# Optimization experiments

Hardware: AMD Instinct MI355X
Metric: run time of the kernel (lower is better)

The kernel has to match this reference:

```python
import jax, jax.numpy as jnp
import numpy as np
from jax import lax

B0, C0, H0, W0 = 4, 128, 48, 48
GR = 32  # growth rate
NL = 4   # dense layers


def conv1x1(x, w, b):
    # w: [O, Cin], x: [B, Cin, H, W]
    return jnp.einsum('oc,bchw->bohw', w, x) + b[None, :, None, None]


def conv3x3(x, w, b):
    y = lax.conv_general_dilated(x, w, (1, 1), [(1, 1), (1, 1)],
                                 dimension_numbers=('NCHW', 'OIHW', 'NCHW'))
    return y + b[None, :, None, None]


def batchnorm(x, g, b, eps=1e-5):
    # training-mode BatchNorm2d: batch statistics over (B, H, W)
    mu = jnp.mean(x, axis=(0, 2, 3), keepdims=True)
    var = jnp.var(x, axis=(0, 2, 3), keepdims=True)
    return (x - mu) * lax.rsqrt(var + eps) * g[None, :, None, None] + b[None, :, None, None]


def apply_rope(x):
    B, C, H, W = x.shape
    half = C // 2
    theta = 1.0 / (10000.0 ** (jnp.arange(half, dtype=x.dtype) / half))
    # pos_emb[h, w, j] = (h + w) * theta[j]
    pos = (jnp.arange(H, dtype=x.dtype)[:, None, None]
           + jnp.arange(W, dtype=x.dtype)[None, :, None]) * theta
    cos = jnp.cos(pos).transpose(2, 0, 1)  # [half, H, W]
    sin = jnp.sin(pos).transpose(2, 0, 1)
    xr = x.reshape(B, half, 2, H, W)
    x_re, x_im = xr[:, :, 0], xr[:, :, 1]
    rr = x_re * cos - x_im * sin
    ri = x_re * sin + x_im * cos
    return jnp.stack([rr, ri], axis=2).reshape(B, C, H, W)


def setup_inputs() -> dict:
    key = jax.random.key(0)
    ks = iter(jax.random.split(key, 64))
    def nrm(shape, s=0.05):
        return jax.random.normal(next(ks), shape, jnp.float32) * s
    C = C0
    dc = C + NL * GR  # 256 dense-block output channels
    hid = 4 * C
    d = {
        'x': jax.random.normal(next(ks), (B0, C0, H0, W0), jnp.float32),
        'r_w': nrm((C, C)), 'r_b': jnp.zeros((C,), jnp.float32),
        'k_w': nrm((C, C)), 'k_b': jnp.zeros((C,), jnp.float32),
        'v_w': nrm((C, C)), 'v_b': jnp.zeros((C,), jnp.float32),
        'wc1_w': nrm((C // 4, C, 3, 3)), 'wc1_b': jnp.zeros((C // 4,), jnp.float32),
        'wc2_w': nrm((C, C // 4)), 'wc2_b': jnp.zeros((C,), jnp.float32),
        'u': nrm((C,), 0.1),
        'sn1_w': nrm((dc // 4, dc)), 'sn1_b': jnp.zeros((dc // 4,), jnp.float32),
        'sn2_w': nrm((dc, dc // 4)), 'sn2_b': jnp.zeros((dc,), jnp.float32),
        'lb_w': nrm((C // 4, dc)), 'lb_b': jnp.zeros((C // 4,), jnp.float32),
        'ld_w': nrm((C // 4, dc)), 'ld_b': jnp.zeros((C // 4,), jnp.float32),
        'ps_w': nrm((C, C // 4)), 'ps_b': jnp.zeros((C,), jnp.float32),
        'pq_w': nrm((C, C)), 'pq_b': jnp.zeros((C,), jnp.float32),
        'fc1_w': nrm((hid, C)), 'fc1_b': jnp.zeros((hid,), jnp.float32),
        'fc2_w': nrm((C, hid)), 'fc2_b': jnp.zeros((C,), jnp.float32),
    }
    for i in range(NL):
        cin = C + i * GR
        d[f'db_g{i}'] = jnp.ones((cin,), jnp.float32)
        d[f'db_b{i}'] = jnp.zeros((cin,), jnp.float32)
        d[f'db_w{i}'] = nrm((GR, cin, 3, 3))
        d[f'db_cb{i}'] = jnp.zeros((GR,), jnp.float32)
    return d


def _forward(x, r_w, r_b, k_w, k_b, v_w, v_b, wc1_w, wc1_b, wc2_w, wc2_b, u,
             db_g0, db_b0, db_w0, db_cb0, db_g1, db_b1, db_w1, db_cb1,
             db_g2, db_b2, db_w2, db_cb2, db_g3, db_b3, db_w3, db_cb3,
             sn1_w, sn1_b, sn2_w, sn2_b, lb_w, lb_b, ld_w, ld_b,
             ps_w, ps_b, pq_w, pq_b, fc1_w, fc1_b, fc2_w, fc2_b):
    B, C, H, W = x.shape
    N = H * W
    # decay gate w (hidden is None so it multiplies zeros, kept for fidelity)
    w_gate = jax.nn.sigmoid(conv1x1(jax.nn.relu(conv3x3(x, wc1_w, wc1_b)), wc2_w, wc2_b)).reshape(B, C, N)
    x_rope = apply_rope(x)
    r = jax.nn.sigmoid(conv1x1(x, r_w, r_b))
    k = conv1x1(x_rope, k_w, k_b).reshape(B, C, N)
    v = conv1x1(x_rope, v_w, v_b).reshape(B, C, N)
    zeros = jnp.zeros_like(k)
    new_num = zeros * jnp.exp(-w_gate) + k * v
    new_den = zeros * jnp.exp(-w_gate) + k
    eu = jnp.exp(u)[None, :, None]
    wkv = ((new_num + eu * k * v) / (new_den + eu * k)).reshape(B, C, H, W)
    recursive_output = r * wkv
    # dense block (concat-growth)
    feats = x
    for g, bb, wt, cb in ((db_g0, db_b0, db_w0, db_cb0), (db_g1, db_b1, db_w1, db_cb1),
                          (db_g2, db_b2, db_w2, db_cb2), (db_g3, db_b3, db_w3, db_cb3)):
        h = jax.nn.relu(batchnorm(feats, g, bb))
        feats = jnp.concatenate([feats, conv3x3(h, wt, cb)], axis=1)
    df = feats  # [B, C+4*GR, H, W]
    # adaptive spiking neuron
    tau = jnp.mean(jax.nn.sigmoid(conv1x1(jax.nn.relu(conv1x1(df, sn1_w, sn1_b)), sn2_w, sn2_b)),
                   axis=(2, 3), keepdims=True)
    spike_prob = jax.nn.sigmoid((df - 1.0) * 5.0)
    sf = spike_prob * (df * jnp.exp(-1.0 / (tau + 1e-6))) + (1.0 - spike_prob) * df
    # first attention over N tokens, channels = C//4
    Bf = conv1x1(sf, lb_w, lb_b).reshape(B, -1, N)
    Df = conv1x1(sf, ld_w, ld_b).reshape(B, -1, N)
    attn = jax.nn.softmax(jnp.einsum('bcn,bcm->bnm', Bf, Bf), axis=-1)
    att1 = jnp.einsum('bnm,bcm->bcn', attn, Df).reshape(B, -1, H, W)
    spike_output = conv1x1(att1, ps_w, ps_b)
    combined = recursive_output + spike_output
    # second attention (k/v convs are shared with WKV path)
    Q = conv1x1(combined, pq_w, pq_b).reshape(B, C, N)
    K = conv1x1(combined, k_w, k_b).reshape(B, C, N)
    V = conv1x1(combined, v_w, v_b).reshape(B, C, N)
    scores = jnp.einsum('bcn,bcm->bnm', Q, K) / jnp.sqrt(jnp.asarray(C, x.dtype))
    aw = jax.nn.softmax(scores, axis=-1)
    att2 = jnp.einsum('bnm,bcm->bcn', aw, V).reshape(B, C, H, W)
    x1 = x + att2
    out = x1 + conv1x1(jax.nn.relu(conv1x1(x1, fc1_w, fc1_b)) ** 2, fc2_w, fc2_b)
    return out, new_num, new_den


def reference(x, r_w, r_b, k_w, k_b, v_w, v_b, wc1_w, wc1_b, wc2_w, wc2_b, u,
              db_g0, db_b0, db_w0, db_cb0, db_g1, db_b1, db_w1, db_cb1,
              db_g2, db_b2, db_w2, db_cb2, db_g3, db_b3, db_w3, db_cb3,
              sn1_w, sn1_b, sn2_w, sn2_b, lb_w, lb_b, ld_w, ld_b,
              ps_w, ps_b, pq_w, pq_b, fc1_w, fc1_b, fc2_w, fc2_b):
    return _forward(x, r_w, r_b, k_w, k_b, v_w, v_b, wc1_w, wc1_b, wc2_w, wc2_b, u,
                    db_g0, db_b0, db_w0, db_cb0, db_g1, db_b1, db_w1, db_cb1,
                    db_g2, db_b2, db_w2, db_cb2, db_g3, db_b3, db_w3, db_cb3,
                    sn1_w, sn1_b, sn2_w, sn2_b, lb_w, lb_b, ld_w, ld_b,
                    ps_w, ps_b, pq_w, pq_b, fc1_w, fc1_b, fc2_w, fc2_b)
```

## Files before the change

kernel.cpp:

```cpp
#include <hip/hip_runtime.h>
#include <math.h>

#define BB 4
#define CC 128
#define HH 48
#define WW 48
#define NSP (HH*WW)
#define DCC 256
#define BCN (BB*CC*NSP)
#define KS 4

typedef float f32x4 __attribute__((ext_vector_type(4)));
typedef __bf16 bf16x8 __attribute__((ext_vector_type(8)));
typedef __bf16 bf16x4 __attribute__((ext_vector_type(4)));

__device__ __forceinline__ float sigmf(float v) { return 1.0f / (1.0f + __expf(-v)); }

struct Prep {
  const float* wsrc[13];
  int wlen[13];
  int woff[13];
  const float* psrc[4];
  int pcin[4];
  int poff[4];
  const float* x;
  float* sums;
  float* sums2;
  __bf16* x_t;
  __bf16* xrope_t;
};
__global__ __launch_bounds__(256) void prep_kernel(Prep a, __bf16* __restrict__ wdst,
                                                   __bf16* __restrict__ pdst) {
  __shared__ float lds[32][33];
  __shared__ float rs[4], rs2[4];
  int g = blockIdx.y;
  int idx = blockIdx.x * 256 + threadIdx.x;
  if (g < 13) {
    if (idx < a.wlen[g]) wdst[a.woff[g] + idx] = (__bf16)a.wsrc[g][idx];
  } else if (g < 17) {
    int L = g - 13;
    int cin = a.pcin[L];
    if (idx < 9 * 32 * cin) {
      int c = idx % cin;
      int o = (idx / cin) % 32;
      int tap = idx / (cin * 32);
      pdst[a.poff[L] + idx] = (__bf16)a.psrc[L][((size_t)o * cin + c) * 9 + tap];
    }
  } else if (g == 17) {
    int c = blockIdx.x;
    if (c >= 128) return;
    float s = 0.f, s2 = 0.f;
    for (int i = threadIdx.x; i < BB * NSP; i += 256) {
      int b = i / NSP, n = i % NSP;
      float v = a.x[((size_t)b * 128 + c) * NSP + n];
      s += v;
      s2 += v * v;
    }
#pragma unroll
    for (int off = 32; off > 0; off >>= 1) {
      s += __shfl_down(s, off);
      s2 += __shfl_down(s2, off);
    }
    int wid = threadIdx.x >> 6;
    if ((threadIdx.x & 63) == 0) { rs[wid] = s; rs2[wid] = s2; }
    __syncthreads();
    if (threadIdx.x == 0) {
      a.sums[c] = rs[0] + rs[1] + rs[2] + rs[3];
      a.sums2[c] = rs2[0] + rs2[1] + rs2[2] + rs2[3];
    }
  } else {
    int T = (g - 18) * 256 + blockIdx.x;
    if (T >= 1152) return;
    int b = T / 288;
    int r = T % 288;
    int c0 = (r / 72) * 32;
    int n0 = (r % 72) * 32;
    int tid = threadIdx.x;
    int nn = tid & 31, cs = tid >> 5;
#pragma unroll
    for (int j = 0; j < 4; ++j) {
      int cc = c0 + cs * 4 + j;
      lds[cs * 4 + j][nn] = a.x[((size_t)b * 128 + cc) * NSP + n0 + nn];
    }
    __syncthreads();
    int c = tid & 31, ns = tid >> 5;
#pragma unroll
    for (int j = 0; j < 4; ++j) {
      int n2 = ns * 4 + j;
      float pv = lds[c][n2];
      a.x_t[((size_t)b * NSP + n0 + n2) * 128 + c0 + c] = (__bf16)pv;
      int gc = c0 + c;
      int i = gc >> 1;
      float re = lds[c & ~1][n2];
      float im = lds[c | 1][n2];
      int n = n0 + n2;
      int h = n / WW, w = n % WW;
      float theta = __expf(-9.2103403719761836f * ((float)i) / 64.0f);
      float pos = (float)(h + w) * theta;
      float cs_ = cosf(pos), sn_ = sinf(pos);
      float vr_ = (gc & 1) ? (re * sn_ + im * cs_) : (re * cs_ - im * sn_);
      a.xrope_t[((size_t)b * NSP + n0 + n2) * 128 + c0 + c] = (__bf16)vr_;
    }
  }
}

__global__ __launch_bounds__(256) void kvr_kernel(
    const __bf16* __restrict__ xrope_t, const __bf16* __restrict__ x_t,
    const __bf16* __restrict__ wk, const __bf16* __restrict__ wvp,
    const __bf16* __restrict__ wr,
    const float* __restrict__ k_b, const float* __restrict__ v_b,
    const float* __restrict__ r_b, const float* __restrict__ u,
    float* __restrict__ kden, float* __restrict__ knum, float* __restrict__ rec) {
  int tid = threadIdx.x;
  int wv = tid >> 6, lane = tid & 63;
  int m15 = lane & 15, quad = lane >> 4;
  int b = blockIdx.y;
  int n0 = blockIdx.x * 16;
  int o0 = wv * 32;
  int n = n0 + m15;
  const __bf16* brr = xrope_t + ((size_t)b * NSP + n) * 128 + quad * 8;
  const __bf16* brx = x_t + ((size_t)b * NSP + n) * 128 + quad * 8;
  const __bf16* ak0 = wk + (size_t)(o0 + m15) * 128 + quad * 8;
  const __bf16* ak1 = wk + (size_t)(o0 + 16 + m15) * 128 + quad * 8;
  const __bf16* av0 = wvp + (size_t)(o0 + m15) * 128 + quad * 8;
  const __bf16* av1 = wvp + (size_t)(o0 + 16 + m15) * 128 + quad * 8;
  const __bf16* ar0 = wr + (size_t)(o0 + m15) * 128 + quad * 8;
  const __bf16* ar1 = wr + (size_t)(o0 + 16 + m15) * 128 + quad * 8;
  f32x4 fk[2], fv[2], fr[2];
#pragma unroll
  for (int t = 0; t < 2; ++t) {
    fk[t] = (f32x4){0.f, 0.f, 0.f, 0.f};
    fv[t] = (f32x4){0.f, 0.f, 0.f, 0.f};
    fr[t] = (f32x4){0.f, 0.f, 0.f, 0.f};
  }
#pragma unroll
  for (int kc = 0; kc < 128; kc += 32) {
    bf16x8 br_ = *(const bf16x8*)(brr + kc);
    bf16x8 bx_ = *(const bf16x8*)(brx + kc);
    fk[0] = __builtin_amdgcn_mfma_f32_16x16x32_bf16(*(const bf16x8*)(ak0 + kc), br_, fk[0], 0, 0, 0);
    fk[1] = __builtin_amdgcn_mfma_f32_16x16x32_bf16(*(const bf16x8*)(ak1 + kc), br_, fk[1], 0, 0, 0);
    fv[0] = __builtin_amdgcn_mfma_f32_16x16x32_bf16(*(const bf16x8*)(av0 + kc), br_, fv[0], 0, 0, 0);
    fv[1] = __builtin_amdgcn_mfma_f32_16x16x32_bf16(*(const bf16x8*)(av1 + kc), br_, fv[1], 0, 0, 0);
    fr[0] = __builtin_amdgcn_mfma_f32_16x16x32_bf16(*(const bf16x8*)(ar0 + kc), bx_, fr[0], 0, 0, 0);
    fr[1] = __builtin_amdgcn_mfma_f32_16x16x32_bf16(*(const bf16x8*)(ar1 + kc), bx_, fr[1], 0, 0, 0);
  }
#pragma unroll
  for (int t = 0; t < 2; ++t) {
#pragma unroll
    for (int reg = 0; reg < 4; ++reg) {
      int ol = o0 + t * 16 + quad * 4 + reg;
      float kk = fk[t][reg] + k_b[ol];
      float vv = fv[t][reg] + v_b[ol];
      float rr = sigmf(fr[t][reg] + r_b[ol]);
      float eu = __expf(u[ol]);
      size_t idx = ((size_t)b * 128 + ol) * NSP + n;
      float nv = kk * vv, tt = eu * kk;
      kden[idx] = kk;
      knum[idx] = nv;
      rec[idx] = rr * ((nv + tt * vv) / (kk + tt));
    }
  }
}

template <int OUT>
__device__ __forceinline__ void gemm_store(void* outp, int b, int n, int Oseg,
                                           int obase, int quad, const float* vr) {
  if (OUT == 0) {
    float* op = (float*)outp;
#pragma unroll
    for (int reg = 0; reg < 4; ++reg)
      op[((size_t)b * Oseg + obase + quad * 4 + reg) * NSP + n] = vr[reg];
  } else if (OUT == 1) {
    __bf16* op = (__bf16*)outp;
    bf16x4 pk;
#pragma unroll
    for (int reg = 0; reg < 4; ++reg) pk[reg] = (__bf16)vr[reg];
    *(bf16x4*)(op + ((size_t)b * NSP + n) * Oseg + obase + quad * 4) = pk;
  } else {
    __bf16* op = (__bf16*)outp;
#pragma unroll
    for (int reg = 0; reg < 4; ++reg)
      op[((size_t)b * Oseg + obase + quad * 4 + reg) * NSP + n] = (__bf16)vr[reg];
  }
}

template <int K, int ACT, int OUT0, int OUT1, int OUT2, int SPLITB>
__global__ __launch_bounds__(256) void gemm_mfma_kernel(
    const __bf16* __restrict__ in_t, const __bf16* __restrict__ in_t2,
    const __bf16* __restrict__ wb,
    const float* __restrict__ bias0, const float* __restrict__ bias1,
    const float* __restrict__ bias2,
    const float* __restrict__ add0, const float* __restrict__ add1,
    void* __restrict__ out0, void* __restrict__ out1, void* __restrict__ out2,
    int osplit, int osplit2, int Ototal, float sc0, float sc1, float sc2) {
  int tid = threadIdx.x;
  int wv = tid >> 6, lane = tid & 63;
  int m15 = lane & 15, quad = lane >> 4;
  int b = blockIdx.y;
  int n0 = blockIdx.x * 16;
  int wpb = blockDim.x >> 6;
  int o0 = (blockIdx.z * wpb + wv) * 32;
  if (o0 >= Ototal) return;
  int n = n0 + m15;
  const __bf16* brow = in_t + ((size_t)b * NSP + n) * (SPLITB ? 128 : K) + quad * 8;
  const __bf16* brow2 = SPLITB ? (in_t2 + ((size_t)b * NSP + n) * 128 + quad * 8) : nullptr;
  const __bf16* a0p = wb + (size_t)(o0 + m15) * K + quad * 8;
  const __bf16* a1p = wb + (size_t)(o0 + 16 + m15) * K + quad * 8;
  f32x4 of0 = (f32x4){0.f, 0.f, 0.f, 0.f};
  f32x4 of1 = (f32x4){0.f, 0.f, 0.f, 0.f};
#pragma unroll
  for (int kc = 0; kc < K; kc += 32) {
    bf16x8 bfr;
    if constexpr (SPLITB) {
      bfr = (kc < 128) ? *(const bf16x8*)(brow + kc) : *(const bf16x8*)(brow2 + (kc - 128));
    } else {
      bfr = *(const bf16x8*)(brow + kc);
    }
    bf16x8 a0 = *(const bf16x8*)(a0p + kc);
    bf16x8 a1 = *(const bf16x8*)(a1p + kc);
    of0 = __builtin_amdgcn_mfma_f32_16x16x32_bf16(a0, bfr, of0, 0, 0, 0);
    of1 = __builtin_amdgcn_mfma_f32_16x16x32_bf16(a1, bfr, of1, 0, 0, 0);
  }
  int seg = (o0 >= osplit2) ? 2 : (o0 >= osplit) ? 1 : 0;
  int segb = (seg == 2) ? osplit2 : (seg == 1) ? osplit : 0;
  int sege = (seg == 2) ? Ototal : (seg == 1) ? osplit2 : osplit;
  int Oseg = sege - segb;
  int ol0 = o0 - segb;
  const float* bias = (seg == 2) ? bias2 : (seg == 1) ? bias1 : bias0;
  const float* add = (seg == 2) ? nullptr : (seg == 1) ? add1 : add0;
  void* outp = (seg == 2) ? out2 : (seg == 1) ? out1 : out0;
  float sc = (seg == 2) ? sc2 : (seg == 1) ? sc1 : sc0;
#pragma unroll
  for (int t = 0; t < 2; ++t) {
    f32x4 acc = t ? of1 : of0;
    float vr[4];
#pragma unroll
    for (int reg = 0; reg < 4; ++reg) {
      int ol = ol0 + t * 16 + quad * 4 + reg;
      float v = acc[reg] + bias[ol];
      if (ACT == 1) v = fmaxf(v, 0.0f);
      else if (ACT == 2) v = sigmf(v);
      else if (ACT == 3) { v = fmaxf(v, 0.0f); v = v * v; }
      v *= sc;
      if (add) v += add[((size_t)b * Oseg + ol) * NSP + n];
      vr[reg] = v;
    }
    if constexpr (OUT0 == 3) {
#pragma unroll
      for (int reg = 0; reg < 4; ++reg) {
        float sv = vr[reg];
        sv += __shfl_xor(sv, 1);
        sv += __shfl_xor(sv, 2);
        sv += __shfl_xor(sv, 4);
        sv += __shfl_xor(sv, 8);
        if (m15 == 0)
          ((float*)out0)[((size_t)(b * DCC + ol0 + t * 16 + quad * 4 + reg)) * 144 +
                         blockIdx.x] = sv;
      }
    } else {
      if (seg == 0) gemm_store<OUT0>(outp, b, n, Oseg, ol0 + t * 16, quad, vr);
      else if (seg == 1) gemm_store<OUT1>(outp, b, n, Oseg, ol0 + t * 16, quad, vr);
      else gemm_store<OUT2>(outp, b, n, Oseg, ol0 + t * 16, quad, vr);
    }
  }
}

__global__ __launch_bounds__(128) void lbld_sf_kernel(
    const __bf16* __restrict__ x_t, const __bf16* __restrict__ dense_t,
    const float* __restrict__ taupart, const __bf16* __restrict__ wlb,
    const float* __restrict__ lb_b, const float* __restrict__ ld_b,
    __bf16* __restrict__ Bft, __bf16* __restrict__ Dfb) {
  __shared__ float ef[256];
  int tid = threadIdx.x;
  int b = blockIdx.y;
  for (int ch = tid; ch < 256; ch += 128) {
    const f32x4* tp = (const f32x4*)(taupart + ((size_t)(b * DCC + ch)) * 144);
    f32x4 s4 = (f32x4){0.f, 0.f, 0.f, 0.f};
#pragma unroll
    for (int j = 0; j < 36; ++j) s4 += tp[j];
    float tv = (s4.x + s4.y + s4.z + s4.w) * (1.0f / (float)NSP);
    ef[ch] = __expf(-1.0f / (tv + 1e-6f)) - 1.0f;
  }
  __syncthreads();
  int wv = tid >> 6, lane = tid & 63;
  int m15 = lane & 15, quad = lane >> 4;
  int n0 = blockIdx.x * 16;
  int o0 = wv * 32;
  int n = n0 + m15;
  const __bf16* bx = x_t + ((size_t)b * NSP + n) * 128 + quad * 8;
  const __bf16* bd = dense_t + ((size_t)b * NSP + n) * 128 + quad * 8;
  const __bf16* a0p = wlb + (size_t)(o0 + m15) * 256 + quad * 8;
  const __bf16* a1p = wlb + (size_t)(o0 + 16 + m15) * 256 + quad * 8;
  f32x4 of0 = (f32x4){0.f, 0.f, 0.f, 0.f};
  f32x4 of1 = (f32x4){0.f, 0.f, 0.f, 0.f};
#pragma unroll
  for (int kc = 0; kc < 256; kc += 32) {
    bf16x8 raw = (kc < 128) ? *(const bf16x8*)(bx + kc) : *(const bf16x8*)(bd + (kc - 128));
    bf16x8 sfv;
#pragma unroll
    for (int j = 0; j < 8; ++j) {
      float df = (float)raw[j];
      float sp = sigmf((df - 1.0f) * 5.0f);
      sfv[j] = (__bf16)(df * (1.0f + sp * ef[kc + quad * 8 + j]));
    }
    bf16x8 a0 = *(const bf16x8*)(a0p + kc);
    bf16x8 a1 = *(const bf16x8*)(a1p + kc);
    of0 = __builtin_amdgcn_mfma_f32_16x16x32_bf16(a0, sfv, of0, 0, 0, 0);
    of1 = __builtin_amdgcn_mfma_f32_16x16x32_bf16(a1, sfv, of1, 0, 0, 0);
  }
  if (o0 == 0) {
#pragma unroll
    for (int t = 0; t < 2; ++t) {
      f32x4 acc = t ? of1 : of0;
      bf16x4 pk;
#pragma unroll
      for (int reg = 0; reg < 4; ++reg) pk[reg] = (__bf16)(acc[reg] + lb_b[t * 16 + quad * 4 + reg]);
      *(bf16x4*)(Bft + ((size_t)b * NSP + n) * 32 + t * 16 + quad * 4) = pk;
    }
  } else {
#pragma unroll
    for (int t = 0; t < 2; ++t) {
      f32x4 acc = t ? of1 : of0;
#pragma unroll
      for (int reg = 0; reg < 4; ++reg) {
        int ol = t * 16 + quad * 4 + reg;
        Dfb[((size_t)b * 32 + ol) * NSP + n] = (__bf16)(acc[reg] + ld_b[ol]);
      }
    }
  }
}

template <int Cin>
__global__ __launch_bounds__(256) void convbn_kernel(
    const __bf16* __restrict__ x_t, const __bf16* __restrict__ dense_t,
    const __bf16* __restrict__ wb, const float* __restrict__ cb,
    float* __restrict__ sums, float* __restrict__ sums2,
    const float* __restrict__ cpart_in,
    const float* __restrict__ g, const float* __restrict__ bbp,
    __bf16* __restrict__ dense_out, float* __restrict__ cpart_out, int cout0) {
  constexpr int KCin = Cin / 32;
  constexpr int NIT = 9 * KCin;
  __shared__ float red[4][64][8];
  __shared__ float scsh[2][Cin];
  __shared__ float tred[64][4];
  __shared__ float fin[64];
  int tid = threadIdx.x;
  const float inv = 1.0f / (float)(BB * NSP);

  if (cpart_in) {
    int row = tid >> 2, sl = tid & 3;
    const f32x4* cp = (const f32x4*)(cpart_in + (size_t)row * 576 + sl * 144);
    f32x4 s4 = (f32x4){0.f, 0.f, 0.f, 0.f};
#pragma unroll
    for (int j = 0; j < 36; ++j) s4 += cp[j];
    tred[row][sl] = s4.x + s4.y + s4.z + s4.w;
    __syncthreads();
    if (tid < 64) fin[tid] = tred[tid][0] + tred[tid][1] + tred[tid][2] + tred[tid][3];
    __syncthreads();
    if (blockIdx.x == 0 && blockIdx.y == 0 && tid < 32) {
      sums[Cin - 32 + tid] = fin[tid];
      sums2[Cin - 32 + tid] = fin[32 + tid];
    }
  }
  for (int ch = tid; ch < Cin; ch += 256) {
    float S, S2;
    if (cpart_in && ch >= Cin - 32) {
      S = fin[ch - (Cin - 32)];
      S2 = fin[ch - (Cin - 32) + 32];
    } else {
      S = sums[ch];
      S2 = sums2[ch];
    }
    float m = S * inv;
    float var = S2 * inv - m * m;
    float sc_ = rsqrtf(var + 1e-5f) * g[ch];
    scsh[0][ch] = sc_;
    scsh[1][ch] = bbp[ch] - m * sc_;
  }
  __syncthreads();

  int wv = tid >> 6, lane = tid & 63;
  int m15 = lane & 15, quad = lane >> 4;
  int b = blockIdx.y;
  int n0 = blockIdx.x * 16;
  int n = n0 + m15;
  int h = n / WW, w = n % WW;
  f32x4 of0 = (f32x4){0.f, 0.f, 0.f, 0.f};
  f32x4 of1 = (f32x4){0.f, 0.f, 0.f, 0.f};
  const __bf16* bx_ = x_t + (size_t)b * NSP * 128;
  const __bf16* bd_ = dense_t + (size_t)b * NSP * 128;
  const bf16x8 zf = {};
  int begin = (wv * NIT) / 4, end = ((wv + 1) * NIT) / 4;
  int cur = -1;
  float bsc[8], bsh[8];
  const __bf16* base = nullptr;
  for (int ci = begin; ci < end; ++ci) {
    int chunk = ci / 9;
    int tap = ci - chunk * 9;
    int kc = chunk * 32;
    if (chunk != cur) {
      cur = chunk;
      int cc = kc + quad * 8;
#pragma unroll
      for (int j = 0; j < 8; ++j) {
        bsc[j] = scsh[0][cc + j];
        bsh[j] = scsh[1][cc + j];
      }
      base = (cc < 128) ? (bx_ + cc) : (bd_ + cc - 128);
    }
    int dh = tap / 3 - 1, dw = tap % 3 - 1;
    bool valid = ((unsigned)(h + dh) < HH) && ((unsigned)(w + dw) < WW);
    int pa = valid ? (n + dh * WW + dw) : 0;
    bf16x8 raw = *(const bf16x8*)(base + (size_t)pa * 128);
    bf16x8 bfr;
#pragma unroll
    for (int j = 0; j < 8; ++j) {
      float v = fmaxf((float)raw[j] * bsc[j] + bsh[j], 0.0f);
      bfr[j] = (__bf16)v;
    }
    if (!valid) bfr = zf;
    const __bf16* wt = wb + (size_t)tap * 32 * Cin + kc + quad * 8;
    bf16x8 a0 = *(const bf16x8*)(wt + (size_t)m15 * Cin);
    bf16x8 a1 = *(const bf16x8*)(wt + (size_t)(16 + m15) * Cin);
    of0 = __builtin_amdgcn_mfma_f32_16x16x32_bf16(a0, bfr, of0, 0, 0, 0);
    of1 = __builtin_amdgcn_mfma_f32_16x16x32_bf16(a1, bfr, of1, 0, 0, 0);
  }
  float* myred = red[wv][lane];
#pragma unroll
  for (int reg = 0; reg < 4; ++reg) {
    myred[reg] = of0[reg];
    myred[4 + reg] = of1[reg];
  }
  __syncthreads();
  if (wv == 0) {
    int dloc = cout0 - 128;
    __bf16* dt = dense_out + ((size_t)b * NSP + n) * 128 + dloc;
    bf16x4 pk0, pk1;
    float sv[4][4];
#pragma unroll
    for (int reg = 0; reg < 4; ++reg) {
      int o = quad * 4 + reg;
      float v0 = red[0][lane][reg] + red[1][lane][reg] + red[2][lane][reg] +
                 red[3][lane][reg] + cb[o];
      float v1 = red[0][lane][4 + reg] + red[1][lane][4 + reg] + red[2][lane][4 + reg] +
                 red[3][lane][4 + reg] + cb[16 + o];
      pk0[reg] = (__bf16)v0;
      pk1[reg] = (__bf16)v1;
      sv[reg][0] = v0;
      sv[reg][1] = v0 * v0;
      sv[reg][2] = v1;
      sv[reg][3] = v1 * v1;
    }
    *(bf16x4*)(dt + quad * 4) = pk0;
    *(bf16x4*)(dt + 16 + quad * 4) = pk1;
    if (cpart_out) {
#pragma unroll
      for (int reg = 0; reg < 4; ++reg) {
        float a0 = sv[reg][0], q0 = sv[reg][1], a1 = sv[reg][2], q1 = sv[reg][3];
#pragma unroll
        for (int mk = 1; mk < 16; mk <<= 1) {
          a0 += __shfl_xor(a0, mk);
          q0 += __shfl_xor(q0, mk);
          a1 += __shfl_xor(a1, mk);
          q1 += __shfl_xor(q1, mk);
        }
        if (m15 == 0) {
          int o = quad * 4 + reg;
          int pidx = blockIdx.y * 144 + blockIdx.x;
          cpart_out[(size_t)o * 576 + pidx] = a0;
          cpart_out[(size_t)(32 + o) * 576 + pidx] = q0;
          cpart_out[(size_t)(16 + o) * 576 + pidx] = a1;
          cpart_out[(size_t)(48 + o) * 576 + pidx] = q1;
        }
      }
    }
  }
}

template <int CD>
__global__ __launch_bounds__(256) void attn_part_kernel(
    const __bf16* __restrict__ Qt, const __bf16* __restrict__ Kt,
    const __bf16* __restrict__ Vb, __bf16* __restrict__ Op,
    float* __restrict__ lp) {
  constexpr int NC = CD / 16;
  constexpr int KC = CD / 32;
  constexpr int KEYS = NSP / KS;
  constexpr int KP = CD + 4;
  constexpr int VP = 36;
  __shared__ __bf16 kl[32][KP];
  __shared__ __bf16 vl[CD][VP];
  __shared__ float pt[4][16][36];
  int tid = threadIdx.x;
  int wv = tid >> 6, lane = tid & 63;
  int m15 = lane & 15, quad = lane >> 4;
  int b = blockIdx.y, ks = blockIdx.z;
  int n0 = blockIdx.x * 64 + wv * 16;

  bf16x8 qf[KC];
  const __bf16* qrow = Qt + ((size_t)b * NSP + n0 + m15) * CD + quad * 8;
#pragma unroll
  for (int kc = 0; kc < KC; ++kc) qf[kc] = *(const bf16x8*)(qrow + kc * 32);

  f32x4 of[NC];
#pragma unroll
  for (int i = 0; i < NC; ++i) of[i] = (f32x4){0.f, 0.f, 0.f, 0.f};
  float l0 = 0.f, l1 = 0.f, l2 = 0.f, l3 = 0.f;

  const __bf16* Kb = Kt + (size_t)b * NSP * CD;
  const __bf16* Vbb = Vb + (size_t)b * CD * NSP;
  float(*ptw)[36] = pt[wv];

  for (int m0 = ks * KEYS; m0 < (ks + 1) * KEYS; m0 += 32) {
    __syncthreads();
    for (int i = tid; i < 32 * CD / 8; i += 256) {
      int row = i / (CD / 8);
      int cc8 = (i % (CD / 8)) * 8;
      *(bf16x8*)&kl[row][cc8] = *(const bf16x8*)(Kb + (size_t)(m0 + row) * CD + cc8);
    }
    for (int i = tid; i < CD * 4; i += 256) {
      int ch = i / 4;
      int k8 = (i % 4) * 8;
      *(bf16x8*)&vl[ch][k8] = *(const bf16x8*)(Vbb + (size_t)ch * NSP + m0 + k8);
    }
    __syncthreads();
    f32x4 s[2];
#pragma unroll
    for (int t = 0; t < 2; ++t) {
      f32x4 acc = (f32x4){0.f, 0.f, 0.f, 0.f};
#pragma unroll
      for (int kc = 0; kc < KC; ++kc) {
        bf16x8 kf = *(const bf16x8*)&kl[t * 16 + m15][kc * 32 + quad * 8];
        acc = __builtin_amdgcn_mfma_f32_16x16x32_bf16(qf[kc], kf, acc, 0, 0, 0);
      }
      s[t] = acc;
    }
#pragma unroll
    for (int t = 0; t < 2; ++t) {
      float e0 = __expf(s[t].x), e1 = __expf(s[t].y), e2 = __expf(s[t].z), e3 = __expf(s[t].w);
      l0 += e0; l1 += e1; l2 += e2; l3 += e3;
      ptw[quad * 4 + 0][t * 16 + m15] = e0;
      ptw[quad * 4 + 1][t * 16 + m15] = e1;
      ptw[quad * 4 + 2][t * 16 + m15] = e2;
      ptw[quad * 4 + 3][t * 16 + m15] = e3;
    }
    const float* prow = &ptw[m15][quad * 8];
    f32x4 pa = *(const f32x4*)(prow);
    f32x4 pb = *(const f32x4*)(prow + 4);
    bf16x8 pf;
    pf[0] = (__bf16)pa.x; pf[1] = (__bf16)pa.y; pf[2] = (__bf16)pa.z; pf[3] = (__bf16)pa.w;
    pf[4] = (__bf16)pb.x; pf[5] = (__bf16)pb.y; pf[6] = (__bf16)pb.z; pf[7] = (__bf16)pb.w;
#pragma unroll
    for (int ct = 0; ct < NC; ++ct) {
      bf16x8 vf = *(const bf16x8*)&vl[ct * 16 + m15][quad * 8];
      of[ct] = __builtin_amdgcn_mfma_f32_16x16x32_bf16(pf, vf, of[ct], 0, 0, 0);
    }
  }

#pragma unroll
  for (int off = 1; off < 16; off <<= 1) {
    l0 += __shfl_xor(l0, off);
    l1 += __shfl_xor(l1, off);
    l2 += __shfl_xor(l2, off);
    l3 += __shfl_xor(l3, off);
  }
  float* lpb = lp + (size_t)(ks * BB + b) * NSP + n0;
  if (m15 == 0) {
    lpb[quad * 4 + 0] = l0;
    lpb[quad * 4 + 1] = l1;
    lpb[quad * 4 + 2] = l2;
    lpb[quad * 4 + 3] = l3;
  }
  __bf16* Ob = Op + (size_t)(ks * BB + b) * CD * NSP;
#pragma unroll
  for (int ct = 0; ct < NC; ++ct) {
    bf16x4 pk;
#pragma unroll
    for (int reg = 0; reg < 4; ++reg) pk[reg] = (__bf16)of[ct][reg];
    *(bf16x4*)(Ob + (size_t)(ct * 16 + m15) * NSP + n0 + quad * 4) = pk;
  }
}

__global__ __launch_bounds__(256) void combine32_kernel(const __bf16* __restrict__ Op,
                                                        const float* __restrict__ lp,
                                                        __bf16* __restrict__ att1_t) {
  __shared__ float lds[32][33];
  int b = blockIdx.z;
  int n0 = blockIdx.x * 32;
  int tid = threadIdx.x;
  int nn = tid & 31, cs = tid >> 5;
  float ltot = 0.f;
#pragma unroll
  for (int ks = 0; ks < KS; ++ks) ltot += lp[(size_t)(ks * BB + b) * NSP + n0 + nn];
  float linv = 1.0f / ltot;
#pragma unroll
  for (int j = 0; j < 4; ++j) {
    int cc = cs * 4 + j;
    float s = 0.f;
#pragma unroll
    for (int ks = 0; ks < KS; ++ks)
      s += (float)Op[((size_t)(ks * BB + b) * 32 + cc) * NSP + n0 + nn];
    lds[cc][nn] = s * linv;
  }
  __syncthreads();
  int c = tid & 31, ns = tid >> 5;
#pragma unroll
  for (int j = 0; j < 4; ++j) {
    int n2 = ns * 4 + j;
    att1_t[((size_t)b * NSP + n0 + n2) * 32 + c] = (__bf16)lds[c][n2];
  }
}

__global__ __launch_bounds__(256) void combine128_kernel(
    const __bf16* __restrict__ Op, const float* __restrict__ lp,
    const float* __restrict__ x, float* __restrict__ x1, __bf16* __restrict__ x1_t) {
  __shared__ float lds[32][33];
  int b = blockIdx.z;
  int n0 = blockIdx.x * 32;
  int c0 = blockIdx.y * 32;
  int tid = threadIdx.x;
  int nn = tid & 31, cs = tid >> 5;
  float ltot = 0.f;
#pragma unroll
  for (int ks = 0; ks < KS; ++ks) ltot += lp[(size_t)(ks * BB + b) * NSP + n0 + nn];
  float linv = 1.0f / ltot;
#pragma unroll
  for (int j = 0; j < 4; ++j) {
    int gc = c0 + cs * 4 + j;
    float s = 0.f;
#pragma unroll
    for (int ks = 0; ks < KS; ++ks)
      s += (float)Op[((size_t)(ks * BB + b) * CC + gc) * NSP + n0 + nn];
    float v = s * linv + x[((size_t)b * CC + gc) * NSP + n0 + nn];
    lds[cs * 4 + j][nn] = v;
    x1[((size_t)b * CC + gc) * NSP + n0 + nn] = v;
  }
  __syncthreads();
  int c = tid & 31, ns = tid >> 5;
#pragma unroll
  for (int j = 0; j < 4; ++j) {
    int n2 = ns * 4 + j;
    x1_t[((size_t)b * NSP + n0 + n2) * CC + c0 + c] = (__bf16)lds[c][n2];
  }
}

extern "C" void kernel_launch(void* const* d_in, const int* in_sizes, int n_in,
                              void* d_out, int out_size, void* d_ws, size_t ws_size,
                              hipStream_t stream) {
  const float* x = (const float*)d_in[0];
  const float* r_w = (const float*)d_in[1];
  const float* r_b = (const float*)d_in[2];
  const float* k_w = (const float*)d_in[3];
  const float* k_b = (const float*)d_in[4];
  const float* v_w = (const float*)d_in[5];
  const float* v_b = (const float*)d_in[6];
  const float* u = (const float*)d_in[11];
  const float* sn1_w = (const float*)d_in[12];
  const float* sn1_b = (const float*)d_in[13];
  const float* sn2_w = (const float*)d_in[14];
  const float* sn2_b = (const float*)d_in[15];
  const float* lb_w = (const float*)d_in[16];
  const float* lb_b = (const float*)d_in[17];
  const float* ld_w = (const float*)d_in[18];
  const float* ld_b = (const float*)d_in[19];
  const float* ps_w = (const float*)d_in[20];
  const float* ps_b = (const float*)d_in[21];
  const float* pq_w = (const float*)d_in[22];
  const float* pq_b = (const float*)d_in[23];
  const float* fc1_w = (const float*)d_in[24];
  const float* fc1_b = (const float*)d_in[25];
  const float* fc2_w = (const float*)d_in[26];
  const float* fc2_b = (const float*)d_in[27];
  const float* db_g[4] = {(const float*)d_in[28], (const float*)d_in[32],
                          (const float*)d_in[36], (const float*)d_in[40]};
  const float* db_b[4] = {(const float*)d_in[29], (const float*)d_in[33],
                          (const float*)d_in[37], (const float*)d_in[41]};
  const float* db_w[4] = {(const float*)d_in[30], (const float*)d_in[34],
                          (const float*)d_in[38], (const float*)d_in[42]};
  const float* db_cb[4] = {(const float*)d_in[31], (const float*)d_in[35],
                           (const float*)d_in[39], (const float*)d_in[43]};

  float* outp = (float*)d_out;
  float* knum = outp + BCN;
  float* kden = outp + 2 * (size_t)BCN;

  float* ws = (float*)d_ws;
  const size_t F_FEATS = 0;
  const size_t F_REC = 4718592;
  const size_t F_V = 5898240;
  const size_t F_R = 7077888;
  const size_t F_XR = 8257536;
  const size_t F_XT = 8847360;
  const size_t F_DFB = 9437184;
  const size_t F_AT1T = 9584640;
  const size_t F_CT = 9732096;
  const size_t F_LP = 10321920;
  const size_t F_WB = 10434048;
  const size_t F_WB3 = 10575360;
  const size_t F_STATS = 10676736;
  const size_t F_TAUP = 10714112;
  float* sums = ws + F_STATS;
  float* sums2 = ws + F_STATS + 256;
  float* cpart0 = ws + F_FEATS;
  float* cpart1 = cpart0 + 36864;
  float* cpart2 = cpart1 + 36864;
  float* taupart = ws + F_TAUP;
  float* lp = ws + F_LP;
  __bf16* wbase = (__bf16*)(ws + F_WB);
  __bf16* wb3 = (__bf16*)(ws + F_WB3);
  const int W_KV = 0;
  const int W_R = 32768;
  const int W_SN1 = 49152;
  const int W_SN2 = 65536;
  const int W_LBLD = 81920;
  const int W_PS = 98304;
  const int W_PQK = 102400;
  const int W_FC1 = 151552;
  const int W_FC2 = 217088;
  const int W3_OFF[4] = {0, 36864, 82944, 138240};

  dim3 blk(256);
  __bf16* xrope_t = (__bf16*)(ws + F_XR);
  __bf16* x_t = (__bf16*)(ws + F_XT);

  Prep pp;
  pp.wsrc[0] = k_w;    pp.wlen[0] = 16384; pp.woff[0] = W_KV;
  pp.wsrc[1] = v_w;    pp.wlen[1] = 16384; pp.woff[1] = W_KV + 16384;
  pp.wsrc[2] = r_w;    pp.wlen[2] = 16384; pp.woff[2] = W_R;
  pp.wsrc[3] = sn1_w;  pp.wlen[3] = 16384; pp.woff[3] = W_SN1;
  pp.wsrc[4] = sn2_w;  pp.wlen[4] = 16384; pp.woff[4] = W_SN2;
  pp.wsrc[5] = lb_w;   pp.wlen[5] = 8192;  pp.woff[5] = W_LBLD;
  pp.wsrc[6] = ld_w;   pp.wlen[6] = 8192;  pp.woff[6] = W_LBLD + 8192;
  pp.wsrc[7] = ps_w;   pp.wlen[7] = 4096;  pp.woff[7] = W_PS;
  pp.wsrc[8] = pq_w;   pp.wlen[8] = 16384; pp.woff[8] = W_PQK;
  pp.wsrc[9] = k_w;    pp.wlen[9] = 16384; pp.woff[9] = W_PQK + 16384;
  pp.wsrc[10] = v_w;   pp.wlen[10] = 16384; pp.woff[10] = W_PQK + 32768;
  pp.wsrc[11] = fc1_w; pp.wlen[11] = 65536; pp.woff[11] = W_FC1;
  pp.wsrc[12] = fc2_w; pp.wlen[12] = 65536; pp.woff[12] = W_FC2;
  for (int i = 0; i < 4; ++i) {
    pp.psrc[i] = db_w[i];
    pp.pcin[i] = 128 + 32 * i;
    pp.poff[i] = W3_OFF[i];
  }
  pp.x = x;
  pp.sums = sums;
  pp.sums2 = sums2;
  pp.x_t = x_t;
  pp.xrope_t = xrope_t;
  prep_kernel<<<dim3(256, 23), blk, 0, stream>>>(pp, wbase, wb3);

  kvr_kernel<<<dim3(144, 4), blk, 0, stream>>>(
      xrope_t, x_t, wbase + W_KV, wbase + W_KV + 16384, wbase + W_R,
      k_b, v_b, r_b, u, kden, knum, ws + F_REC);

  __bf16* dense_t = (__bf16*)(ws + F_R);
  convbn_kernel<128><<<dim3(144, 4), blk, 0, stream>>>(
      x_t, dense_t, wb3 + W3_OFF[0], db_cb[0], sums, sums2, nullptr,
      db_g[0], db_b[0], dense_t, cpart0, 128);
  convbn_kernel<160><<<dim3(144, 4), blk, 0, stream>>>(
      x_t, dense_t, wb3 + W3_OFF[1], db_cb[1], sums, sums2, cpart0,
      db_g[1], db_b[1], dense_t, cpart1, 160);
  convbn_kernel<192><<<dim3(144, 4), blk, 0, stream>>>(
      x_t, dense_t, wb3 + W3_OFF[2], db_cb[2], sums, sums2, cpart1,
      db_g[2], db_b[2], dense_t, cpart2, 192);
  convbn_kernel<224><<<dim3(144, 4), blk, 0, stream>>>(
      x_t, dense_t, wb3 + W3_OFF[3], db_cb[3], sums, sums2, cpart2,
      db_g[3], db_b[3], dense_t, nullptr, 224);

  __bf16* z1_t = (__bf16*)(ws + F_XR);
  gemm_mfma_kernel<256, 1, 1, 1, 0, 1><<<dim3(144, 4, 1), dim3(128), 0, stream>>>(
      x_t, dense_t, wbase + W_SN1, sn1_b, sn1_b, nullptr, nullptr, nullptr,
      z1_t, z1_t, nullptr, 64, 64, 64, 1.f, 1.f, 1.f);
  gemm_mfma_kernel<64, 2, 3, 3, 0, 0><<<dim3(144, 4, 2), blk, 0, stream>>>(
      z1_t, nullptr, wbase + W_SN2, sn2_b, sn2_b, nullptr, nullptr, nullptr,
      taupart, taupart, nullptr, 256, 256, 256, 1.f, 1.f, 1.f);
  __bf16* Bft = (__bf16*)(ws + F_CT + 294912);
  __bf16* Dfb = (__bf16*)(ws + F_DFB);
  lbld_sf_kernel<<<dim3(144, 4), dim3(128), 0, stream>>>(
      x_t, dense_t, taupart, wbase + W_LBLD, lb_b, ld_b, Bft, Dfb);
  __bf16* Opart = (__bf16*)(ws + F_FEATS);
  attn_part_kernel<32><<<dim3(36, 4, KS), blk, 0, stream>>>(Bft, Bft, Dfb, Opart, lp);
  __bf16* att1_t = (__bf16*)(ws + F_AT1T);
  combine32_kernel<<<dim3(72, 1, 4), blk, 0, stream>>>(Opart, lp, att1_t);
  __bf16* comb_t = (__bf16*)(ws + F_CT);
  gemm_mfma_kernel<32, 0, 1, 1, 0, 0><<<dim3(144, 4, 1), blk, 0, stream>>>(
      att1_t, nullptr, wbase + W_PS, ps_b, ps_b, nullptr, ws + F_REC, ws + F_REC,
      comb_t, comb_t, nullptr, 128, 128, 128, 1.f, 1.f, 1.f);

  __bf16* Qt = (__bf16*)(ws + F_XR);
  __bf16* K2t = (__bf16*)(ws + F_XT);
  __bf16* V2b = (__bf16*)(ws + F_V);
  gemm_mfma_kernel<128, 0, 1, 1, 2, 0><<<dim3(144, 4, 3), blk, 0, stream>>>(
      comb_t, nullptr, wbase + W_PQK, pq_b, k_b, v_b, nullptr, nullptr,
      Qt, K2t, V2b, 128, 256, 384, 0.08838834764831845f, 1.f, 1.f);
  attn_part_kernel<128><<<dim3(36, 4, KS), blk, 0, stream>>>(Qt, K2t, V2b, Opart, lp);
  float* x1 = ws + F_R;
  __bf16* x1_t = (__bf16*)(ws + F_CT);
  combine128_kernel<<<dim3(72, 4, 4), blk, 0, stream>>>(Opart, lp, x, x1, x1_t);

  __bf16* h_t = (__bf16*)(ws + F_FEATS);
  gemm_mfma_kernel<128, 3, 1, 1, 0, 0><<<dim3(144, 4, 4), blk, 0, stream>>>(
      x1_t, nullptr, wbase + W_FC1, fc1_b, fc1_b, nullptr, nullptr, nullptr,
      h_t, h_t, nullptr, 512, 512, 512, 1.f, 1.f, 1.f);
  gemm_mfma_kernel<512, 0, 0, 0, 0, 0><<<dim3(144, 4, 1), blk, 0, stream>>>(
      h_t, nullptr, wbase + W_FC2, fc2_b, fc2_b, nullptr, x1, x1,
      outp, outp, nullptr, 128, 128, 128, 1.f, 1.f, 1.f);
}
```

Measured before the change: 413.6 us.

## Double-buffer K/V tiles with register prefetch and double key splits in attention

```diff
diff --git a/kernel.cpp b/kernel.cpp
--- a/kernel.cpp
+++ b/kernel.cpp
@@ -8,7 +8,7 @@
 #define NSP (HH*WW)
 #define DCC 256
 #define BCN (BB*CC*NSP)
-#define KS 4
+#define KS 8
 
 typedef float f32x4 __attribute__((ext_vector_type(4)));
 typedef __bf16 bf16x8 __attribute__((ext_vector_type(8)));
@@ -485,11 +485,13 @@
   constexpr int NC = CD / 16;
   constexpr int KC = CD / 32;
   constexpr int KEYS = NSP / KS;
-  constexpr int KP = CD + 4;
-  constexpr int VP = 36;
-  __shared__ __bf16 kl[32][KP];
-  __shared__ __bf16 vl[CD][VP];
-  __shared__ float pt[4][16][36];
+  constexpr int NT = KEYS / 32;
+  constexpr int KP = CD + 2;
+  constexpr int VP = 34;
+  constexpr int NST = CD / 32;
+  __shared__ __bf16 kl[2][32][KP];
+  __shared__ __bf16 vl[2][CD][VP];
+  __shared__ __bf16 ptb[4][16][40];
   int tid = threadIdx.x;
   int wv = tid >> 6, lane = tid & 63;
   int m15 = lane & 15, quad = lane >> 4;
@@ -508,28 +510,63 @@
 
   const __bf16* Kb = Kt + (size_t)b * NSP * CD;
   const __bf16* Vbb = Vb + (size_t)b * CD * NSP;
-  float(*ptw)[36] = pt[wv];
-
-  for (int m0 = ks * KEYS; m0 < (ks + 1) * KEYS; m0 += 32) {
-    __syncthreads();
-    for (int i = tid; i < 32 * CD / 8; i += 256) {
-      int row = i / (CD / 8);
-      int cc8 = (i % (CD / 8)) * 8;
-      *(bf16x8*)&kl[row][cc8] = *(const bf16x8*)(Kb + (size_t)(m0 + row) * CD + cc8);
-    }
-    for (int i = tid; i < CD * 4; i += 256) {
-      int ch = i / 4;
-      int k8 = (i % 4) * 8;
-      *(bf16x8*)&vl[ch][k8] = *(const bf16x8*)(Vbb + (size_t)ch * NSP + m0 + k8);
-    }
-    __syncthreads();
+
+  {
+    int m0 = ks * KEYS;
+    bf16x8 st[NST];
+#pragma unroll
+    for (int j = 0; j < NST; ++j) {
+      int c = tid + j * 256;
+      if (c < 4 * CD) {
+        int row = c / (CD / 8), c8 = (c % (CD / 8)) * 8;
+        st[j] = *(const bf16x8*)(Kb + (size_t)(m0 + row) * CD + c8);
+      } else {
+        int c2 = c - 4 * CD;
+        int ch = c2 >> 2, k8 = (c2 & 3) * 8;
+        st[j] = *(const bf16x8*)(Vbb + (size_t)ch * NSP + m0 + k8);
+      }
+    }
+#pragma unroll
+    for (int j = 0; j < NST; ++j) {
+      int c = tid + j * 256;
+      if (c < 4 * CD) {
+        int row = c / (CD / 8), c8 = (c % (CD / 8)) * 8;
+        *(bf16x8*)&kl[0][row][c8] = st[j];
+      } else {
+        int c2 = c - 4 * CD;
+        int ch = c2 >> 2, k8 = (c2 & 3) * 8;
+        *(bf16x8*)&vl[0][ch][k8] = st[j];
+      }
+    }
+  }
+  __syncthreads();
+
+  for (int it = 0; it < NT; ++it) {
+    int cur = it & 1;
+    bool more = (it + 1 < NT);
+    bf16x8 st[NST];
+    if (more) {
+      int m0n = ks * KEYS + (it + 1) * 32;
+#pragma unroll
+      for (int j = 0; j < NST; ++j) {
+        int c = tid + j * 256;
+        if (c < 4 * CD) {
+          int row = c / (CD / 8), c8 = (c % (CD / 8)) * 8;
+          st[j] = *(const bf16x8*)(Kb + (size_t)(m0n + row) * CD + c8);
+        } else {
+          int c2 = c - 4 * CD;
+          int ch = c2 >> 2, k8 = (c2 & 3) * 8;
+          st[j] = *(const bf16x8*)(Vbb + (size_t)ch * NSP + m0n + k8);
+        }
+      }
+    }
     f32x4 s[2];
 #pragma unroll
     for (int t = 0; t < 2; ++t) {
       f32x4 acc = (f32x4){0.f, 0.f, 0.f, 0.f};
 #pragma unroll
       for (int kc = 0; kc < KC; ++kc) {
-        bf16x8 kf = *(const bf16x8*)&kl[t * 16 + m15][kc * 32 + quad * 8];
+        bf16x8 kf = *(const bf16x8*)&kl[cur][t * 16 + m15][kc * 32 + quad * 8];
         acc = __builtin_amdgcn_mfma_f32_16x16x32_bf16(qf[kc], kf, acc, 0, 0, 0);
       }
       s[t] = acc;
@@ -538,22 +575,32 @@
     for (int t = 0; t < 2; ++t) {
       float e0 = __expf(s[t].x), e1 = __expf(s[t].y), e2 = __expf(s[t].z), e3 = __expf(s[t].w);
       l0 += e0; l1 += e1; l2 += e2; l3 += e3;
-      ptw[quad * 4 + 0][t * 16 + m15] = e0;
-      ptw[quad * 4 + 1][t * 16 + m15] = e1;
-      ptw[quad * 4 + 2][t * 16 + m15] = e2;
-      ptw[quad * 4 + 3][t * 16 + m15] = e3;
-    }
-    const float* prow = &ptw[m15][quad * 8];
-    f32x4 pa = *(const f32x4*)(prow);
-    f32x4 pb = *(const f32x4*)(prow + 4);
-    bf16x8 pf;
-    pf[0] = (__bf16)pa.x; pf[1] = (__bf16)pa.y; pf[2] = (__bf16)pa.z; pf[3] = (__bf16)pa.w;
-    pf[4] = (__bf16)pb.x; pf[5] = (__bf16)pb.y; pf[6] = (__bf16)pb.z; pf[7] = (__bf16)pb.w;
+      ptb[wv][quad * 4 + 0][t * 16 + m15] = (__bf16)e0;
+      ptb[wv][quad * 4 + 1][t * 16 + m15] = (__bf16)e1;
+      ptb[wv][quad * 4 + 2][t * 16 + m15] = (__bf16)e2;
+      ptb[wv][quad * 4 + 3][t * 16 + m15] = (__bf16)e3;
+    }
+    bf16x8 pf = *(const bf16x8*)&ptb[wv][m15][quad * 8];
 #pragma unroll
     for (int ct = 0; ct < NC; ++ct) {
-      bf16x8 vf = *(const bf16x8*)&vl[ct * 16 + m15][quad * 8];
+      bf16x8 vf = *(const bf16x8*)&vl[cur][ct * 16 + m15][quad * 8];
       of[ct] = __builtin_amdgcn_mfma_f32_16x16x32_bf16(pf, vf, of[ct], 0, 0, 0);
     }
+    if (more) {
+#pragma unroll
+      for (int j = 0; j < NST; ++j) {
+        int c = tid + j * 256;
+        if (c < 4 * CD) {
+          int row = c / (CD / 8), c8 = (c % (CD / 8)) * 8;
+          *(bf16x8*)&kl[cur ^ 1][row][c8] = st[j];
+        } else {
+          int c2 = c - 4 * CD;
+          int ch = c2 >> 2, k8 = (c2 & 3) * 8;
+          *(bf16x8*)&vl[cur ^ 1][ch][k8] = st[j];
+        }
+      }
+    }
+    __syncthreads();
   }
 
 #pragma unroll
```

Result: slower. 426.2 us (+3.1%).
